# Performance work log

Measured on AMD Instinct MI355X. Metric: run time of the kernel, lower is better.

Reference implementation:

```python
import jax, jax.numpy as jnp
import numpy as np

VOCAB = 50257
N_TURNS = 4
POLY_DEGREE = 3
OUT_DIM = 128
BATCH, SEQ = 32, 8192


def setup_inputs() -> dict:
    key = jax.random.key(0)
    k1, k2, k3 = jax.random.split(key, 3)
    token_ids = jax.random.randint(k1, (BATCH, SEQ), 0, VOCAB, dtype=jnp.int32)
    # original init: randint(-5, 6).float()
    turns = jax.random.randint(k2, (VOCAB, N_TURNS), -5, 6).astype(jnp.float32)
    poly_coeffs = jax.random.normal(k3, (N_TURNS, POLY_DEGREE + 1, OUT_DIM), dtype=jnp.float32) * 0.1
    return {"token_ids": token_ids, "turns": turns, "poly_coeffs": poly_coeffs}


def reference(token_ids, turns, poly_coeffs):
    # gather turn vectors: (b, s, n_turns)
    base_turns = turns[token_ids]
    P = poly_coeffs.shape[1]  # poly_degree + 1
    # powers x^0..x^degree for every turn: (b, s, n_turns, P)
    powers = base_turns[..., None] ** jnp.arange(P, dtype=base_turns.dtype)
    # sum over turns of einsum('bsp,po->bso') == single fused contraction
    return jnp.einsum('bstp,tpo->bso', powers, poly_coeffs)
```

## Files before the change

### kernel.cpp

```cpp
#include <hip/hip_runtime.h>


constexpr int N_TOKENS = 32 * 8192;
constexpr int OUT_DIM  = 128;
constexpr int N_TURNS  = 4;
constexpr int P        = 4;

constexpr int BLOCK         = 256;
constexpr int TOK_PER_ITER  = BLOCK / 32;
constexpr int GRID          = 2048;
constexpr int TOK_PER_BLOCK = N_TOKENS / GRID;
constexpr int ITERS         = TOK_PER_BLOCK / TOK_PER_ITER;

__device__ __forceinline__ float4 f4_fma(float a, const float4 b, const float4 c) {
    return make_float4(fmaf(a, b.x, c.x),
                       fmaf(a, b.y, c.y),
                       fmaf(a, b.z, c.z),
                       fmaf(a, b.w, c.w));
}

__device__ __forceinline__ float4 f4_add(const float4 a, const float4 b) {
    return make_float4(a.x + b.x, a.y + b.y, a.z + b.z, a.w + b.w);
}

__global__ __launch_bounds__(BLOCK) void TurnEmbedding_50053548867731_kernel(
    const int*    __restrict__ token_ids,
    const float4* __restrict__ turns,
    const float*  __restrict__ coeffs,
    float4*       __restrict__ out)
{
    const int tid  = threadIdx.x;
    const int slot = tid >> 5;
    const int o4   = tid & 31;

    float4 c[N_TURNS][P];
#pragma unroll
    for (int t = 0; t < N_TURNS; ++t)
#pragma unroll
        for (int p = 0; p < P; ++p)
            c[t][p] = *reinterpret_cast<const float4*>(coeffs + (t * P + p) * OUT_DIM + o4 * 4);

    const int base = blockIdx.x * TOK_PER_BLOCK + slot;

#pragma unroll 2
    for (int it = 0; it < ITERS; ++it) {
        const int tok = base + it * TOK_PER_ITER;

        const int id = token_ids[tok];
        const float4 x4 = turns[id];

        float xs[N_TURNS] = {x4.x, x4.y, x4.z, x4.w};

        float4 acc = make_float4(0.f, 0.f, 0.f, 0.f);
#pragma unroll
        for (int t = 0; t < N_TURNS; ++t) {
            const float x = xs[t];
            float4 r = f4_fma(x, c[t][3], c[t][2]);
            r = f4_fma(x, r, c[t][1]);
            r = f4_fma(x, r, c[t][0]);
            acc = f4_add(acc, r);
        }

        out[tok * (OUT_DIM / 4) + o4] = acc;
    }
}

extern "C" void kernel_launch(void* const* d_in, const int* in_sizes, int n_in,
                              void* d_out, int out_size, void* d_ws, size_t ws_size,
                              hipStream_t stream) {
    const int*   token_ids = (const int*)d_in[0];
    const float* turns     = (const float*)d_in[1];
    const float* coeffs    = (const float*)d_in[2];
    float*       out       = (float*)d_out;

    TurnEmbedding_50053548867731_kernel<<<GRID, BLOCK, 0, stream>>>(
        token_ids,
        reinterpret_cast<const float4*>(turns),
        coeffs,
        reinterpret_cast<float4*>(out));
}
```

Before: 155.7 us.

## Batch gathers per thread group, fold constant coefficients, use nontemporal stores

Each thread now issues eight token-id loads, then eight turn-vector gathers, before computing, so more memory requests are in flight at once. The constant terms of all turns are summed once into the accumulator's starting value, which removes one FMA and the add per turn. Output writes use nontemporal stores to limit cache pollution from the large streaming output. The cost is higher register pressure from the fully unrolled loop and the grouped buffers.

```diff
diff --git a/kernel.cpp b/kernel.cpp
--- a/kernel.cpp
+++ b/kernel.cpp
@@ -4,64 +4,76 @@
 constexpr int N_TOKENS = 32 * 8192;
 constexpr int OUT_DIM  = 128;
 constexpr int N_TURNS  = 4;
-constexpr int P        = 4;
 
 constexpr int BLOCK         = 256;
 constexpr int TOK_PER_ITER  = BLOCK / 32;
 constexpr int GRID          = 2048;
 constexpr int TOK_PER_BLOCK = N_TOKENS / GRID;
 constexpr int ITERS         = TOK_PER_BLOCK / TOK_PER_ITER;
+constexpr int GROUP         = 8;
 
-__device__ __forceinline__ float4 f4_fma(float a, const float4 b, const float4 c) {
-    return make_float4(fmaf(a, b.x, c.x),
-                       fmaf(a, b.y, c.y),
-                       fmaf(a, b.z, c.z),
-                       fmaf(a, b.w, c.w));
-}
+typedef float floatx4 __attribute__((ext_vector_type(4)));
 
-__device__ __forceinline__ float4 f4_add(const float4 a, const float4 b) {
-    return make_float4(a.x + b.x, a.y + b.y, a.z + b.z, a.w + b.w);
+__device__ __forceinline__ floatx4 f4_fma(float a, const floatx4 b, const floatx4 c) {
+    floatx4 r;
+    r.x = fmaf(a, b.x, c.x);
+    r.y = fmaf(a, b.y, c.y);
+    r.z = fmaf(a, b.z, c.z);
+    r.w = fmaf(a, b.w, c.w);
+    return r;
 }
 
 __global__ __launch_bounds__(BLOCK) void TurnEmbedding_50053548867731_kernel(
-    const int*    __restrict__ token_ids,
-    const float4* __restrict__ turns,
-    const float*  __restrict__ coeffs,
-    float4*       __restrict__ out)
+    const int*     __restrict__ token_ids,
+    const floatx4* __restrict__ turns,
+    const float*   __restrict__ coeffs,
+    floatx4*       __restrict__ out)
 {
     const int tid  = threadIdx.x;
     const int slot = tid >> 5;
     const int o4   = tid & 31;
 
-    float4 c[N_TURNS][P];
+    floatx4 c1[N_TURNS], c2[N_TURNS], c3[N_TURNS];
+    floatx4 c0sum = (floatx4)(0.f);
 #pragma unroll
-    for (int t = 0; t < N_TURNS; ++t)
-#pragma unroll
-        for (int p = 0; p < P; ++p)
-            c[t][p] = *reinterpret_cast<const float4*>(coeffs + (t * P + p) * OUT_DIM + o4 * 4);
+    for (int t = 0; t < N_TURNS; ++t) {
+        const float* base_t = coeffs + (t * 4) * OUT_DIM + o4 * 4;
+        c0sum = c0sum + *reinterpret_cast<const floatx4*>(base_t + 0 * OUT_DIM);
+        c1[t] = *reinterpret_cast<const floatx4*>(base_t + 1 * OUT_DIM);
+        c2[t] = *reinterpret_cast<const floatx4*>(base_t + 2 * OUT_DIM);
+        c3[t] = *reinterpret_cast<const floatx4*>(base_t + 3 * OUT_DIM);
+    }
 
     const int base = blockIdx.x * TOK_PER_BLOCK + slot;
 
-#pragma unroll 2
-    for (int it = 0; it < ITERS; ++it) {
-        const int tok = base + it * TOK_PER_ITER;
+#pragma unroll
+    for (int g = 0; g < ITERS / GROUP; ++g) {
+        int ids[GROUP];
+#pragma unroll
+        for (int i = 0; i < GROUP; ++i)
+            ids[i] = token_ids[base + (g * GROUP + i) * TOK_PER_ITER];
 
-        const int id = token_ids[tok];
-        const float4 x4 = turns[id];
+        floatx4 xs[GROUP];
+#pragma unroll
+        for (int i = 0; i < GROUP; ++i)
+            xs[i] = turns[ids[i]];
 
-        float xs[N_TURNS] = {x4.x, x4.y, x4.z, x4.w};
+#pragma unroll
+        for (int i = 0; i < GROUP; ++i) {
+            const int tok = base + (g * GROUP + i) * TOK_PER_ITER;
+            const float xv[N_TURNS] = {xs[i].x, xs[i].y, xs[i].z, xs[i].w};
 
-        float4 acc = make_float4(0.f, 0.f, 0.f, 0.f);
+            floatx4 acc = c0sum;
 #pragma unroll
-        for (int t = 0; t < N_TURNS; ++t) {
-            const float x = xs[t];
-            float4 r = f4_fma(x, c[t][3], c[t][2]);
-            r = f4_fma(x, r, c[t][1]);
-            r = f4_fma(x, r, c[t][0]);
-            acc = f4_add(acc, r);
+            for (int t = 0; t < N_TURNS; ++t) {
+                const float x = xv[t];
+                floatx4 r = f4_fma(x, c3[t], c2[t]);
+                r = f4_fma(x, r, c1[t]);
+                acc = f4_fma(x, r, acc);
+            }
+
+            __builtin_nontemporal_store(acc, &out[tok * (OUT_DIM / 4) + o4]);
         }
-
-        out[tok * (OUT_DIM / 4) + o4] = acc;
     }
 }
 
@@ -71,11 +83,10 @@
     const int*   token_ids = (const int*)d_in[0];
     const float* turns     = (const float*)d_in[1];
     const float* coeffs    = (const float*)d_in[2];
-    float*       out       = (float*)d_out;
 
     TurnEmbedding_50053548867731_kernel<<<GRID, BLOCK, 0, stream>>>(
         token_ids,
-        reinterpret_cast<const float4*>(turns),
+        reinterpret_cast<const floatx4*>(turns),
         coeffs,
-        reinterpret_cast<float4*>(out));
+        reinterpret_cast<floatx4*>(d_out));
 }
```

New measurement: 153.3 us. No clear change (-1.5%).
